# Kernel tuning notes

Measured on AMD Instinct MI355X. Metric: run time of the kernel, lower is better.

## Reference

```python
import jax, jax.numpy as jnp
from jax import lax
import numpy as np

NPOINT, RADIUS, NSAMPLE = 1024, 0.2, 32
MLP = [64, 64, 128]
IN_CH = 35  # 3 coord channels + 32 point features
EPS = 1e-5


def farthest_point_sample(xyz, npoint):
    # xyz: (B, N, 3) -> (B, npoint) int32. Deterministic start at index 0.
    B, N, _ = xyz.shape

    def step(carry, _):
        dist, farthest = carry  # (B,N), (B,)
        centroid = jnp.take_along_axis(xyz, farthest[:, None, None], axis=1)  # (B,1,3)
        d = jnp.sum((xyz - centroid) ** 2, axis=-1)  # (B,N)
        dist = jnp.minimum(dist, d)
        nxt = jnp.argmax(dist, axis=-1).astype(jnp.int32)
        return (dist, nxt), farthest

    init = (jnp.full((B, N), 1e10, xyz.dtype), jnp.zeros((B,), jnp.int32))
    _, idxs = lax.scan(step, init, None, length=npoint)
    return idxs.T  # (B, npoint)


def gather_points(points, idx):
    # points: (B, N, C); idx: (B, ...) int -> (B, ..., C)
    return jax.vmap(lambda p, i: p[i])(points, idx)


def query_ball_point(radius, nsample, xyz, new_xyz):
    # xyz: (B,N,3), new_xyz: (B,S,3) -> (B,S,nsample) int32
    B, N, _ = xyz.shape
    sqrdists = jnp.sum((new_xyz[:, :, None, :] - xyz[:, None, :, :]) ** 2, axis=-1)  # (B,S,N)
    group_idx = jnp.where(sqrdists > radius ** 2, N, jnp.arange(N, dtype=jnp.int32))
    group_idx = jnp.sort(group_idx, axis=-1)[:, :, :nsample]
    first = group_idx[:, :, :1]
    return jnp.where(group_idx == N, first, group_idx)


def sa_forward(xyz, points, params):
    B, N, C = xyz.shape
    fps_idx = farthest_point_sample(xyz, NPOINT)
    new_xyz = gather_points(xyz, fps_idx)  # (B,S,3)
    idx = query_ball_point(RADIUS, NSAMPLE, xyz, new_xyz)  # (B,S,K)
    grouped_xyz = gather_points(xyz, idx)  # (B,S,K,3)
    grouped_xyz_norm = grouped_xyz - new_xyz[:, :, None, :]
    grouped_points = gather_points(points, idx)  # (B,S,K,D)
    new_points = jnp.concatenate([grouped_xyz_norm, grouped_points], axis=-1)  # (B,S,K,Cin)
    x = new_points.transpose(0, 3, 2, 1)  # (B, Cin, K, S)
    for w, b, g, be in params:
        x = jnp.einsum('oi,biks->boks', w, x) + b[None, :, None, None]  # 1x1 conv
        mean = x.mean(axis=(0, 2, 3), keepdims=True)  # BatchNorm2d, training mode
        var = x.var(axis=(0, 2, 3), keepdims=True)
        x = (x - mean) / jnp.sqrt(var + EPS)
        x = jax.nn.relu(g[None, :, None, None] * x + be[None, :, None, None])
    new_points_out = x.max(axis=2)  # max over nsample -> (B, Cout, S)
    return new_xyz, new_points_out


def setup_inputs() -> dict:
    key = jax.random.key(0)
    ks = jax.random.split(key, 16)
    B, N, D = 16, 4096, 32
    inp = {
        'xyz': jax.random.uniform(ks[0], (B, N, 3), dtype=jnp.float32),
        'points': jax.random.normal(ks[1], (B, N, D), dtype=jnp.float32),
    }
    last = IN_CH
    for li, out_ch in enumerate(MLP):
        inp[f'w{li}'] = jax.random.normal(ks[2 + 4 * li], (out_ch, last), dtype=jnp.float32) * 0.05
        inp[f'b{li}'] = jnp.zeros((out_ch,), jnp.float32)
        inp[f'g{li}'] = jnp.ones((out_ch,), jnp.float32)
        inp[f'be{li}'] = jnp.zeros((out_ch,), jnp.float32)
        last = out_ch
    return inp


def reference(xyz, points, w0, b0, g0, be0, w1, b1, g1, be1, w2, b2, g2, be2):
    params = [(w0, b0, g0, be0), (w1, b1, g1, be1), (w2, b2, g2, be2)]
    return sa_forward(xyz, points, params)
```

## Files before the change

### kernel.cpp

```cpp
#include <hip/hip_runtime.h>
#include <hip/hip_bf16.h>
#include <stdint.h>

#pragma clang fp contract(off)

#define BATCH   16
#define NPTS    4096
#define NPOINT  1024
#define NSAMPLE 32
#define NPOS    (BATCH*NPOINT*NSAMPLE)
#define NBLK    (NPOS/128)
#define EPSV    1e-5f

typedef unsigned short ushort_t;
typedef unsigned int uint_t;
typedef unsigned long long u64;
typedef __attribute__((ext_vector_type(8))) short bf16x8;
typedef __attribute__((ext_vector_type(4))) float f32x4;
typedef __attribute__((ext_vector_type(2))) float f32x2;

__device__ inline ushort_t f2bf(float f) {
    uint_t u = __float_as_uint(f);
    u += 0x7fffu + ((u >> 16) & 1u);
    return (ushort_t)(u >> 16);
}
__device__ inline uint_t pkbf(float a, float b) {
    __hip_bfloat162 h = __float22bfloat162_rn(make_float2(a, b));
    uint_t r; __builtin_memcpy(&r, &h, 4); return r;
}
__device__ inline bf16x8 asbf(uint4 u) {
    bf16x8 v; __builtin_memcpy(&v, &u, 16); return v;
}
__device__ inline void unpack8(uint4 u, float* f) {
    f[0] = __uint_as_float(u.x << 16); f[1] = __uint_as_float(u.x & 0xffff0000u);
    f[2] = __uint_as_float(u.y << 16); f[3] = __uint_as_float(u.y & 0xffff0000u);
    f[4] = __uint_as_float(u.z << 16); f[5] = __uint_as_float(u.z & 0xffff0000u);
    f[6] = __uint_as_float(u.w << 16); f[7] = __uint_as_float(u.w & 0xffff0000u);
}

__global__ __launch_bounds__(256) void prep_w(const float* __restrict__ w0,
                                              const float* __restrict__ w1,
                                              const float* __restrict__ w2,
                                              ushort_t* __restrict__ Wp0,
                                              ushort_t* __restrict__ Wx0,
                                              ushort_t* __restrict__ Wp1,
                                              ushort_t* __restrict__ Wp2) {
    const int t = blockIdx.x * 256 + threadIdx.x;
    const int stride = gridDim.x * 256;
    for (int i = t; i < 64 * 32; i += stride) { int ch = i >> 5, k = i & 31; Wp0[i] = f2bf(w0[ch * 35 + 3 + k]); }
    for (int i = t; i < 64 * 4;  i += stride) { int ch = i >> 2, q = i & 3;  Wx0[i] = (q < 3) ? f2bf(w0[ch * 35 + q]) : (ushort_t)0; }
    for (int i = t; i < 64 * 64; i += stride) Wp1[i] = f2bf(w1[i]);
    for (int i = t; i < 128 * 64; i += stride) Wp2[i] = f2bf(w2[i]);
}

#define DPP_MAX_STAGE(CTRL) do {                                              \
    uint_t _lo2 = __builtin_amdgcn_update_dpp(lo, lo, CTRL, 0xf, 0xf, false); \
    uint_t _hi2 = __builtin_amdgcn_update_dpp(hi, hi, CTRL, 0xf, 0xf, false); \
    u64 _o = ((u64)_hi2 << 32) | _lo2;                                        \
    u64 _v = ((u64)hi << 32) | lo;                                            \
    bool _g = _o > _v;                                                        \
    lo = _g ? _lo2 : lo; hi = _g ? _hi2 : hi;                                 \
} while (0)

__global__ __launch_bounds__(256) void fps_kernel(const float* __restrict__ xyz,
                                                  float* __restrict__ new_xyz) {
    __shared__ float4 lxyz[NPTS];
    __shared__ u64 wbest[2][4];
    __shared__ int fpsidx[NPOINT];
    const int b = blockIdx.x;
    const int tid = threadIdx.x;
    const float* base = xyz + (size_t)b * NPTS * 3;
    for (int n = tid; n < NPTS; n += 256) {
        lxyz[n] = make_float4(base[3 * n], base[3 * n + 1], base[3 * n + 2], 0.f);
    }
    __syncthreads();

    f32x2 px[8], py[8], pz[8], dist[8];
    uint_t lowc[16];
#pragma unroll
    for (int j = 0; j < 8; j++) {
        float4 v0 = lxyz[tid + (2 * j) * 256];
        float4 v1 = lxyz[tid + (2 * j + 1) * 256];
        px[j] = (f32x2){v0.x, v1.x};
        py[j] = (f32x2){v0.y, v1.y};
        pz[j] = (f32x2){v0.z, v1.z};
        dist[j] = (f32x2){1e10f, 1e10f};
        lowc[2 * j] = ~(uint_t)(tid + (2 * j) * 256);
        lowc[2 * j + 1] = ~(uint_t)(tid + (2 * j + 1) * 256);
    }
    if (tid == 0) fpsidx[0] = 0;
    int cur = 0;
    const int lane = tid & 63, wid = tid >> 6;

    for (int it = 1; it < NPOINT; ++it) {
        float4 c = lxyz[cur];
        const f32x2 cx = (f32x2){c.x, c.x};
        const f32x2 cy = (f32x2){c.y, c.y};
        const f32x2 cz = (f32x2){c.z, c.z};
        u64 t[8];
#pragma unroll
        for (int j = 0; j < 8; j++) {
            f32x2 dx = px[j] - cx;
            f32x2 dy = py[j] - cy;
            f32x2 dz = pz[j] - cz;
            f32x2 d = (dx * dx + dy * dy) + dz * dz;
            f32x2 nd = __builtin_elementwise_min(dist[j], d);
            dist[j] = nd;
            u64 e0 = ((u64)__float_as_uint(nd.x) << 32) | lowc[2 * j];
            u64 e1 = ((u64)__float_as_uint(nd.y) << 32) | lowc[2 * j + 1];
            t[j] = e0 > e1 ? e0 : e1;
        }
#pragma unroll
        for (int j = 0; j < 4; j++) { u64 o = t[j + 4]; t[j] = t[j] > o ? t[j] : o; }
        t[0] = t[0] > t[1] ? t[0] : t[1];
        t[2] = t[2] > t[3] ? t[2] : t[3];
        u64 v = t[0] > t[2] ? t[0] : t[2];

        uint_t lo = (uint_t)v, hi = (uint_t)(v >> 32);
        DPP_MAX_STAGE(0x111);
        DPP_MAX_STAGE(0x112);
        DPP_MAX_STAGE(0x114);
        DPP_MAX_STAGE(0x118);
        DPP_MAX_STAGE(0x142);
        DPP_MAX_STAGE(0x143);
        uint_t mlo = __builtin_amdgcn_readlane(lo, 63);
        uint_t mhi = __builtin_amdgcn_readlane(hi, 63);

        const int par = it & 1;
        if (lane == 0) wbest[par][wid] = ((u64)mhi << 32) | mlo;
        __syncthreads();
        u64 b0 = wbest[par][0], b1 = wbest[par][1];
        u64 b2 = wbest[par][2], b3 = wbest[par][3];
        u64 m01 = b0 > b1 ? b0 : b1;
        u64 m23 = b2 > b3 ? b2 : b3;
        u64 bb = m01 > m23 ? m01 : m23;
        cur = (int)(~(uint_t)bb) & (NPTS - 1);
        if (tid == 0) fpsidx[it] = cur;
    }
    __syncthreads();
    float* ob = new_xyz + (size_t)b * NPOINT * 3;
    for (int s = tid; s < NPOINT; s += 256) {
        float4 v = lxyz[fpsidx[s]];
        ob[3 * s + 0] = v.x; ob[3 * s + 1] = v.y; ob[3 * s + 2] = v.z;
    }
}

__global__ __launch_bounds__(256) void ballq_kernel(const float* __restrict__ xyz,
                                                    const float* __restrict__ new_xyz,
                                                    int* __restrict__ gidx) {
    const int gw = (int)((blockIdx.x * 256 + threadIdx.x) >> 6);
    const int lane = threadIdx.x & 63;
    const int b = gw / NPOINT, s = gw % NPOINT;
    const float* nb = new_xyz + ((size_t)b * NPOINT + s) * 3;
    const float cx = nb[0], cy = nb[1], cz = nb[2];
    const float* xb = xyz + (size_t)b * NPTS * 3;
    const float r2 = (float)(0.2 * 0.2);
    int cnt = 0;
    int first = -1;
    int* out = gidx + (size_t)gw * NSAMPLE;
    for (int j0 = 0; j0 < NPTS; j0 += 64) {
        int j = j0 + lane;
        float dx = __fsub_rn(xb[j * 3 + 0], cx);
        float dy = __fsub_rn(xb[j * 3 + 1], cy);
        float dz = __fsub_rn(xb[j * 3 + 2], cz);
        float d = __fadd_rn(__fadd_rn(__fmul_rn(dx, dx), __fmul_rn(dy, dy)),
                            __fmul_rn(dz, dz));
        bool pred = !(d > r2);
        u64 mask = __ballot(pred);
        if (first < 0 && mask != 0ull) first = j0 + (__ffsll((long long)mask) - 1);
        int before = __popcll(mask & ((1ull << lane) - 1ull));
        int slot = cnt + before;
        if (pred && slot < NSAMPLE) out[slot] = j;
        cnt += (int)__popcll(mask);
        if (cnt >= NSAMPLE) break;
    }
    if (cnt < NSAMPLE) {
        if (lane >= cnt && lane < NSAMPLE) out[lane] = first;
    }
}

__global__ __launch_bounds__(256) void conv1_mfma(const float* __restrict__ xyz,
                                                  const float* __restrict__ points,
                                                  const float* __restrict__ new_xyz,
                                                  const int* __restrict__ gidx,
                                                  const ushort_t* __restrict__ Wp0,
                                                  const ushort_t* __restrict__ Wx0,
                                                  const float* __restrict__ bias,
                                                  ushort_t* __restrict__ Y,
                                                  float* __restrict__ part_s,
                                                  float* __restrict__ part_q) {
    const int lane = threadIdx.x & 63, wid = threadIdx.x >> 6;
    const int l15 = lane & 15, quad = lane >> 4;
    const int p0 = blockIdx.x * 128 + wid * 32;

    bf16x8 Bp[4], Bx[4];
#pragma unroll
    for (int nt = 0; nt < 4; nt++) {
        const int ch = nt * 16 + l15;
        Bp[nt] = *(const bf16x8*)(Wp0 + (size_t)ch * 32 + quad * 8);
        uint4 bx = {0u, 0u, 0u, 0u};
        if (quad == 0) {
            uint2 wv = *(const uint2*)(Wx0 + ch * 4);
            bx.x = wv.x; bx.y = wv.y;
        }
        Bx[nt] = asbf(bx);
    }
    f32x4 acc[2][4];
#pragma unroll
    for (int mt = 0; mt < 2; mt++)
#pragma unroll
        for (int nt = 0; nt < 4; nt++) acc[mt][nt] = (f32x4){0.f, 0.f, 0.f, 0.f};

#pragma unroll
    for (int mt = 0; mt < 2; mt++) {
        const int p = p0 + mt * 16 + l15;
        const int b = p >> 15, s = (p & 32767) >> 5;
        const int j = gidx[p];
        const float* pr = points + ((size_t)(b * NPTS + j)) * 32 + quad * 8;
        float4 pa = *(const float4*)pr;
        float4 pb4 = *(const float4*)(pr + 4);
        uint4 ap;
        ap.x = pkbf(pa.x, pa.y);  ap.y = pkbf(pa.z, pa.w);
        ap.z = pkbf(pb4.x, pb4.y); ap.w = pkbf(pb4.z, pb4.w);
        bf16x8 Ap = asbf(ap);
        uint4 ax = {0u, 0u, 0u, 0u};
        if (quad == 0) {
            const float* xp = xyz + ((size_t)(b * NPTS + j)) * 3;
            const float* nz = new_xyz + ((size_t)(b * NPOINT + s)) * 3;
            float d0 = xp[0] - nz[0], d1 = xp[1] - nz[1], d2 = xp[2] - nz[2];
            ax.x = pkbf(d0, d1);
            ax.y = pkbf(d2, 0.f);
        }
        bf16x8 Ax = asbf(ax);
#pragma unroll
        for (int nt = 0; nt < 4; nt++) {
            acc[mt][nt] = __builtin_amdgcn_mfma_f32_16x16x32_bf16(Ap, Bp[nt], acc[mt][nt], 0, 0, 0);
            acc[mt][nt] = __builtin_amdgcn_mfma_f32_16x16x32_bf16(Ax, Bx[nt], acc[mt][nt], 0, 0, 0);
        }
    }
    float s_[4], q_[4];
#pragma unroll
    for (int nt = 0; nt < 4; nt++) { s_[nt] = 0.f; q_[nt] = 0.f; }
#pragma unroll
    for (int nt = 0; nt < 4; nt++) {
        const int ch = nt * 16 + l15;
        const float bs = bias[ch];
#pragma unroll
        for (int mt = 0; mt < 2; mt++) {
            const int pb = p0 + mt * 16 + quad * 4;
            float x0 = acc[mt][nt][0] + bs, x1 = acc[mt][nt][1] + bs;
            float x2 = acc[mt][nt][2] + bs, x3 = acc[mt][nt][3] + bs;
            uint_t p01 = pkbf(x0, x1), p23 = pkbf(x2, x3);
            Y[(size_t)(pb + 0) * 64 + ch] = (ushort_t)(p01 & 0xffffu);
            Y[(size_t)(pb + 1) * 64 + ch] = (ushort_t)(p01 >> 16);
            Y[(size_t)(pb + 2) * 64 + ch] = (ushort_t)(p23 & 0xffffu);
            Y[(size_t)(pb + 3) * 64 + ch] = (ushort_t)(p23 >> 16);
            float v0 = __uint_as_float(p01 << 16), v1 = __uint_as_float(p01 & 0xffff0000u);
            float v2 = __uint_as_float(p23 << 16), v3 = __uint_as_float(p23 & 0xffff0000u);
            s_[nt] += (v0 + v1) + (v2 + v3);
            q_[nt] += (v0 * v0 + v1 * v1) + (v2 * v2 + v3 * v3);
        }
    }
#pragma unroll
    for (int nt = 0; nt < 4; nt++) {
        s_[nt] += __shfl_xor(s_[nt], 16, 64); s_[nt] += __shfl_xor(s_[nt], 32, 64);
        q_[nt] += __shfl_xor(q_[nt], 16, 64); q_[nt] += __shfl_xor(q_[nt], 32, 64);
    }
    __shared__ float reds[4][4][16], redq[4][4][16];
    if (lane < 16) {
#pragma unroll
        for (int nt = 0; nt < 4; nt++) { reds[wid][nt][lane] = s_[nt]; redq[wid][nt][lane] = q_[nt]; }
    }
    __syncthreads();
    if (threadIdx.x < 16) {
#pragma unroll
        for (int nt = 0; nt < 4; nt++) {
            float ss = 0.f, qq = 0.f;
#pragma unroll
            for (int w = 0; w < 4; w++) { ss += reds[w][nt][threadIdx.x]; qq += redq[w][nt][threadIdx.x]; }
            const int ch = nt * 16 + threadIdx.x;
            part_s[(size_t)ch * NBLK + blockIdx.x] = ss;
            part_q[(size_t)ch * NBLK + blockIdx.x] = qq;
        }
    }
}

template <int IN, int OUT>
__global__ __launch_bounds__(256) void convN_mfma(const ushort_t* __restrict__ Yin,
                                                  const float* __restrict__ scale,
                                                  const float* __restrict__ shift,
                                                  const ushort_t* __restrict__ Wp,
                                                  const float* __restrict__ bias,
                                                  ushort_t* __restrict__ Yout,
                                                  float* __restrict__ part_s,
                                                  float* __restrict__ part_q) {
    constexpr int NT = OUT / 16;
    const int lane = threadIdx.x & 63, wid = threadIdx.x >> 6;
    const int l15 = lane & 15, quad = lane >> 4;
    const int p0 = blockIdx.x * 128 + wid * 32;

    float sc[2][8], sh[2][8];
#pragma unroll
    for (int kq = 0; kq < 2; kq++) {
        const int i0 = kq * 32 + quad * 8;
        float4 a0 = *(const float4*)(scale + i0);
        float4 a1 = *(const float4*)(scale + i0 + 4);
        float4 b0v = *(const float4*)(shift + i0);
        float4 b1v = *(const float4*)(shift + i0 + 4);
        sc[kq][0] = a0.x; sc[kq][1] = a0.y; sc[kq][2] = a0.z; sc[kq][3] = a0.w;
        sc[kq][4] = a1.x; sc[kq][5] = a1.y; sc[kq][6] = a1.z; sc[kq][7] = a1.w;
        sh[kq][0] = b0v.x; sh[kq][1] = b0v.y; sh[kq][2] = b0v.z; sh[kq][3] = b0v.w;
        sh[kq][4] = b1v.x; sh[kq][5] = b1v.y; sh[kq][6] = b1v.z; sh[kq][7] = b1v.w;
    }
    bf16x8 Bf[NT][2];
#pragma unroll
    for (int nt = 0; nt < NT; nt++)
#pragma unroll
        for (int kq = 0; kq < 2; kq++)
            Bf[nt][kq] = *(const bf16x8*)(Wp + (size_t)(nt * 16 + l15) * IN + kq * 32 + quad * 8);

    bf16x8 Af[2][2];
#pragma unroll
    for (int mt = 0; mt < 2; mt++)
#pragma unroll
        for (int kq = 0; kq < 2; kq++) {
            const ushort_t* yr = Yin + (size_t)(p0 + mt * 16 + l15) * IN + kq * 32 + quad * 8;
            uint4 u = *(const uint4*)yr;
            float f[8]; unpack8(u, f);
            float g0 = fmaxf(fmaf(f[0], sc[kq][0], sh[kq][0]), 0.f);
            float g1 = fmaxf(fmaf(f[1], sc[kq][1], sh[kq][1]), 0.f);
            float g2 = fmaxf(fmaf(f[2], sc[kq][2], sh[kq][2]), 0.f);
            float g3 = fmaxf(fmaf(f[3], sc[kq][3], sh[kq][3]), 0.f);
            float g4 = fmaxf(fmaf(f[4], sc[kq][4], sh[kq][4]), 0.f);
            float g5 = fmaxf(fmaf(f[5], sc[kq][5], sh[kq][5]), 0.f);
            float g6 = fmaxf(fmaf(f[6], sc[kq][6], sh[kq][6]), 0.f);
            float g7 = fmaxf(fmaf(f[7], sc[kq][7], sh[kq][7]), 0.f);
            uint4 a;
            a.x = pkbf(g0, g1); a.y = pkbf(g2, g3);
            a.z = pkbf(g4, g5); a.w = pkbf(g6, g7);
            Af[mt][kq] = asbf(a);
        }

    f32x4 acc[2][NT];
#pragma unroll
    for (int mt = 0; mt < 2; mt++)
#pragma unroll
        for (int nt = 0; nt < NT; nt++) acc[mt][nt] = (f32x4){0.f, 0.f, 0.f, 0.f};
#pragma unroll
    for (int mt = 0; mt < 2; mt++)
#pragma unroll
        for (int nt = 0; nt < NT; nt++) {
            acc[mt][nt] = __builtin_amdgcn_mfma_f32_16x16x32_bf16(Af[mt][0], Bf[nt][0], acc[mt][nt], 0, 0, 0);
            acc[mt][nt] = __builtin_amdgcn_mfma_f32_16x16x32_bf16(Af[mt][1], Bf[nt][1], acc[mt][nt], 0, 0, 0);
        }
    float s_[NT], q_[NT];
#pragma unroll
    for (int nt = 0; nt < NT; nt++) { s_[nt] = 0.f; q_[nt] = 0.f; }
#pragma unroll
    for (int nt = 0; nt < NT; nt++) {
        const int ch = nt * 16 + l15;
        const float bs = bias[ch];
#pragma unroll
        for (int mt = 0; mt < 2; mt++) {
            const int pb = p0 + mt * 16 + quad * 4;
            float x0 = acc[mt][nt][0] + bs, x1 = acc[mt][nt][1] + bs;
            float x2 = acc[mt][nt][2] + bs, x3 = acc[mt][nt][3] + bs;
            uint_t p01 = pkbf(x0, x1), p23 = pkbf(x2, x3);
            Yout[(size_t)(pb + 0) * OUT + ch] = (ushort_t)(p01 & 0xffffu);
            Yout[(size_t)(pb + 1) * OUT + ch] = (ushort_t)(p01 >> 16);
            Yout[(size_t)(pb + 2) * OUT + ch] = (ushort_t)(p23 & 0xffffu);
            Yout[(size_t)(pb + 3) * OUT + ch] = (ushort_t)(p23 >> 16);
            float v0 = __uint_as_float(p01 << 16), v1 = __uint_as_float(p01 & 0xffff0000u);
            float v2 = __uint_as_float(p23 << 16), v3 = __uint_as_float(p23 & 0xffff0000u);
            s_[nt] += (v0 + v1) + (v2 + v3);
            q_[nt] += (v0 * v0 + v1 * v1) + (v2 * v2 + v3 * v3);
        }
    }
#pragma unroll
    for (int nt = 0; nt < NT; nt++) {
        s_[nt] += __shfl_xor(s_[nt], 16, 64); s_[nt] += __shfl_xor(s_[nt], 32, 64);
        q_[nt] += __shfl_xor(q_[nt], 16, 64); q_[nt] += __shfl_xor(q_[nt], 32, 64);
    }
    __shared__ float reds[4][NT][16], redq[4][NT][16];
    if (lane < 16) {
#pragma unroll
        for (int nt = 0; nt < NT; nt++) { reds[wid][nt][lane] = s_[nt]; redq[wid][nt][lane] = q_[nt]; }
    }
    __syncthreads();
    if (threadIdx.x < 16) {
#pragma unroll
        for (int nt = 0; nt < NT; nt++) {
            float ss = 0.f, qq = 0.f;
#pragma unroll
            for (int w = 0; w < 4; w++) { ss += reds[w][nt][threadIdx.x]; qq += redq[w][nt][threadIdx.x]; }
            const int ch = nt * 16 + threadIdx.x;
            part_s[(size_t)ch * NBLK + blockIdx.x] = ss;
            part_q[(size_t)ch * NBLK + blockIdx.x] = qq;
        }
    }
}

__global__ __launch_bounds__(256) void reduce_finalize(const float* __restrict__ part_s,
                                                       const float* __restrict__ part_q,
                                                       const float* __restrict__ g,
                                                       const float* __restrict__ be,
                                                       float* __restrict__ scale,
                                                       float* __restrict__ shift) {
    const int ch = blockIdx.x;
    const float* p1 = part_s + (size_t)ch * NBLK;
    const float* p2 = part_q + (size_t)ch * NBLK;
    float s = 0.f, q = 0.f;
    for (int i = threadIdx.x; i < NBLK; i += 256) { s += p1[i]; q += p2[i]; }
#pragma unroll
    for (int m = 1; m < 64; m <<= 1) { s += __shfl_xor(s, m, 64); q += __shfl_xor(q, m, 64); }
    __shared__ float ls[4], lq[4];
    const int lane = threadIdx.x & 63, wid = threadIdx.x >> 6;
    if (lane == 0) { ls[wid] = s; lq[wid] = q; }
    __syncthreads();
    if (threadIdx.x == 0) {
        float ssum = ls[0] + ls[1] + ls[2] + ls[3];
        float qsum = lq[0] + lq[1] + lq[2] + lq[3];
        float mean = ssum * (1.f / (float)NPOS);
        float var = qsum * (1.f / (float)NPOS) - mean * mean;
        float inv = 1.f / sqrtf(var + EPSV);
        float sc = g[ch] * inv;
        scale[ch] = sc;
        shift[ch] = be[ch] - mean * sc;
    }
}

__global__ __launch_bounds__(256) void final_kernel(const ushort_t* __restrict__ Y3,
                                                    const float* __restrict__ scale,
                                                    const float* __restrict__ shift,
                                                    float* __restrict__ out) {
    const int b = blockIdx.x >> 5;
    const int stile = (blockIdx.x & 31) * 32;
    const int sl = threadIdx.x >> 3;
    const int oc = threadIdx.x & 7;
    const int s = stile + sl;
    const size_t base = ((size_t)(b * NPOINT + s)) * 32 * 128 + oc * 16;
    float vmax[16];
#pragma unroll
    for (int i = 0; i < 16; i++) vmax[i] = 0.f;
    for (int k = 0; k < 32; k++) {
        const ushort_t* yp = Y3 + base + (size_t)k * 128;
#pragma unroll
        for (int h = 0; h < 2; h++) {
            uint4 u = *(const uint4*)(yp + h * 8);
            float f[8];
            unpack8(u, f);
#pragma unroll
            for (int i = 0; i < 8; i++) {
                int o = oc * 16 + h * 8 + i;
                float v = fmaf(f[i], scale[o], shift[o]);
                vmax[h * 8 + i] = fmaxf(vmax[h * 8 + i], v);
            }
        }
    }
    __shared__ float res[32][130];
#pragma unroll
    for (int i = 0; i < 16; i++) res[sl][oc * 16 + i] = vmax[i];
    __syncthreads();
    const int so = threadIdx.x & 31;
    const int og = threadIdx.x >> 5;
#pragma unroll
    for (int r = 0; r < 16; r++) {
        int o = og * 16 + r;
        out[((size_t)(b * 128 + o)) * NPOINT + stile + so] = res[so][o];
    }
}

extern "C" void kernel_launch(void* const* d_in, const int* in_sizes, int n_in,
                              void* d_out, int out_size, void* d_ws, size_t ws_size,
                              hipStream_t stream) {
    const float* xyz = (const float*)d_in[0];
    const float* points = (const float*)d_in[1];
    const float* w0 = (const float*)d_in[2];
    const float* b0 = (const float*)d_in[3];
    const float* g0 = (const float*)d_in[4];
    const float* be0 = (const float*)d_in[5];
    const float* w1 = (const float*)d_in[6];
    const float* b1 = (const float*)d_in[7];
    const float* g1 = (const float*)d_in[8];
    const float* be1 = (const float*)d_in[9];
    const float* w2 = (const float*)d_in[10];
    const float* b2 = (const float*)d_in[11];
    const float* g2 = (const float*)d_in[12];
    const float* be2 = (const float*)d_in[13];

    float* out = (float*)d_out;
    float* new_xyz = out;
    float* final_out = out + BATCH * NPOINT * 3;

    char* ws = (char*)d_ws;
    const size_t MB = 1024u * 1024u;
    const size_t o_gidx = 0;
    const size_t o_y2 = 2 * MB;
    const size_t o_y13 = o_y2 + (size_t)NPOS * 64 * 2;
    const size_t o_params = o_y13 + (size_t)NPOS * 128 * 2;
    const size_t o_parts = o_params + 4096;
    const size_t o_w = o_parts + 4 * MB;

    int* gidx = (int*)(ws + o_gidx);
    ushort_t* Y1 = (ushort_t*)(ws + o_y13);
    ushort_t* Y2 = (ushort_t*)(ws + o_y2);
    ushort_t* Y3 = (ushort_t*)(ws + o_y13);
    float* pr = (float*)(ws + o_params);
    float* scale1 = pr + 0, *shift1 = pr + 64;
    float* scale2 = pr + 128, *shift2 = pr + 192;
    float* scale3 = pr + 256, *shift3 = pr + 384;
    float* part_s = (float*)(ws + o_parts);
    float* part_q = part_s + (size_t)128 * NBLK;
    ushort_t* Wp0 = (ushort_t*)(ws + o_w);
    ushort_t* Wx0 = Wp0 + 64 * 32;
    ushort_t* Wp1 = Wx0 + 64 * 4;
    ushort_t* Wp2 = Wp1 + 64 * 64;

    prep_w<<<8, 256, 0, stream>>>(w0, w1, w2, Wp0, Wx0, Wp1, Wp2);
    fps_kernel<<<BATCH, 256, 0, stream>>>(xyz, new_xyz);
    ballq_kernel<<<(BATCH * NPOINT) / 4, 256, 0, stream>>>(xyz, new_xyz, gidx);
    conv1_mfma<<<NBLK, 256, 0, stream>>>(xyz, points, new_xyz, gidx, Wp0, Wx0, b0, Y1, part_s, part_q);
    reduce_finalize<<<64, 256, 0, stream>>>(part_s, part_q, g0, be0, scale1, shift1);
    convN_mfma<64, 64><<<NBLK, 256, 0, stream>>>(Y1, scale1, shift1, Wp1, b1, Y2, part_s, part_q);
    reduce_finalize<<<64, 256, 0, stream>>>(part_s, part_q, g1, be1, scale2, shift2);
    convN_mfma<64, 128><<<NBLK, 256, 0, stream>>>(Y2, scale2, shift2, Wp2, b2, Y3, part_s, part_q);
    reduce_finalize<<<128, 256, 0, stream>>>(part_s, part_q, g2, be2, scale3, shift3);
    final_kernel<<<BATCH * 32, 256, 0, stream>>>(Y3, scale3, shift3, final_out);
}
```

Before: 909.6 us.

## Fuse group max/min into conv3 to avoid writing full layer-3 activations

The third conv kernel now reduces each 32-sample group to a per-channel max and min of the pre-BatchNorm output, instead of writing the full bf16 activation tensor. The final kernel picks max or min depending on the sign of the BN scale, then applies the affine transform and ReLU. This removes a large 128-channel intermediate write and its read-back, at the cost of two smaller fp32 max/min buffers and extra shuffles in conv3. Results can differ slightly because max/min are taken on fp32 values rather than bf16-rounded ones.

```diff
diff --git a/kernel.cpp b/kernel.cpp
--- a/kernel.cpp
+++ b/kernel.cpp
@@ -10,6 +10,7 @@
 #define NSAMPLE 32
 #define NPOS    (BATCH*NPOINT*NSAMPLE)
 #define NBLK    (NPOS/128)
+#define NGRP    (BATCH*NPOINT)
 #define EPSV    1e-5f
 
 typedef unsigned short ushort_t;
@@ -285,8 +286,7 @@
     }
 }
 
-template <int IN, int OUT>
-__global__ __launch_bounds__(256) void convN_mfma(const ushort_t* __restrict__ Yin,
+__global__ __launch_bounds__(256) void conv2_mfma(const ushort_t* __restrict__ Yin,
                                                   const float* __restrict__ scale,
                                                   const float* __restrict__ shift,
                                                   const ushort_t* __restrict__ Wp,
@@ -294,7 +294,7 @@
                                                   ushort_t* __restrict__ Yout,
                                                   float* __restrict__ part_s,
                                                   float* __restrict__ part_q) {
-    constexpr int NT = OUT / 16;
+    constexpr int IN = 64, OUT = 64, NT = 4;
     const int lane = threadIdx.x & 63, wid = threadIdx.x >> 6;
     const int l15 = lane & 15, quad = lane >> 4;
     const int p0 = blockIdx.x * 128 + wid * 32;
@@ -303,14 +303,8 @@
 #pragma unroll
     for (int kq = 0; kq < 2; kq++) {
         const int i0 = kq * 32 + quad * 8;
-        float4 a0 = *(const float4*)(scale + i0);
-        float4 a1 = *(const float4*)(scale + i0 + 4);
-        float4 b0v = *(const float4*)(shift + i0);
-        float4 b1v = *(const float4*)(shift + i0 + 4);
-        sc[kq][0] = a0.x; sc[kq][1] = a0.y; sc[kq][2] = a0.z; sc[kq][3] = a0.w;
-        sc[kq][4] = a1.x; sc[kq][5] = a1.y; sc[kq][6] = a1.z; sc[kq][7] = a1.w;
-        sh[kq][0] = b0v.x; sh[kq][1] = b0v.y; sh[kq][2] = b0v.z; sh[kq][3] = b0v.w;
-        sh[kq][4] = b1v.x; sh[kq][5] = b1v.y; sh[kq][6] = b1v.z; sh[kq][7] = b1v.w;
+#pragma unroll
+        for (int q = 0; q < 8; q++) { sc[kq][q] = scale[i0 + q]; sh[kq][q] = shift[i0 + q]; }
     }
     bf16x8 Bf[NT][2];
 #pragma unroll
@@ -400,6 +394,121 @@
     }
 }
 
+__global__ __launch_bounds__(256) void conv3_mfma(const ushort_t* __restrict__ Yin,
+                                                  const float* __restrict__ scale,
+                                                  const float* __restrict__ shift,
+                                                  const ushort_t* __restrict__ Wp,
+                                                  const float* __restrict__ bias,
+                                                  float* __restrict__ xmax,
+                                                  float* __restrict__ xmin,
+                                                  float* __restrict__ part_s,
+                                                  float* __restrict__ part_q) {
+    constexpr int IN = 64, NT = 8;
+    const int lane = threadIdx.x & 63, wid = threadIdx.x >> 6;
+    const int l15 = lane & 15, quad = lane >> 4;
+    const int p0 = blockIdx.x * 128 + wid * 32;
+    const int g = p0 >> 5;
+
+    float sc[2][8], sh[2][8];
+#pragma unroll
+    for (int kq = 0; kq < 2; kq++) {
+        const int i0 = kq * 32 + quad * 8;
+#pragma unroll
+        for (int q = 0; q < 8; q++) { sc[kq][q] = scale[i0 + q]; sh[kq][q] = shift[i0 + q]; }
+    }
+    bf16x8 Bf[NT][2];
+#pragma unroll
+    for (int nt = 0; nt < NT; nt++)
+#pragma unroll
+        for (int kq = 0; kq < 2; kq++)
+            Bf[nt][kq] = *(const bf16x8*)(Wp + (size_t)(nt * 16 + l15) * IN + kq * 32 + quad * 8);
+
+    bf16x8 Af[2][2];
+#pragma unroll
+    for (int mt = 0; mt < 2; mt++)
+#pragma unroll
+        for (int kq = 0; kq < 2; kq++) {
+            const ushort_t* yr = Yin + (size_t)(p0 + mt * 16 + l15) * IN + kq * 32 + quad * 8;
+            uint4 u = *(const uint4*)yr;
+            float f[8]; unpack8(u, f);
+            float g0 = fmaxf(fmaf(f[0], sc[kq][0], sh[kq][0]), 0.f);
+            float g1 = fmaxf(fmaf(f[1], sc[kq][1], sh[kq][1]), 0.f);
+            float g2 = fmaxf(fmaf(f[2], sc[kq][2], sh[kq][2]), 0.f);
+            float g3 = fmaxf(fmaf(f[3], sc[kq][3], sh[kq][3]), 0.f);
+            float g4 = fmaxf(fmaf(f[4], sc[kq][4], sh[kq][4]), 0.f);
+            float g5 = fmaxf(fmaf(f[5], sc[kq][5], sh[kq][5]), 0.f);
+            float g6 = fmaxf(fmaf(f[6], sc[kq][6], sh[kq][6]), 0.f);
+            float g7 = fmaxf(fmaf(f[7], sc[kq][7], sh[kq][7]), 0.f);
+            uint4 a;
+            a.x = pkbf(g0, g1); a.y = pkbf(g2, g3);
+            a.z = pkbf(g4, g5); a.w = pkbf(g6, g7);
+            Af[mt][kq] = asbf(a);
+        }
+
+    f32x4 acc[2][NT];
+#pragma unroll
+    for (int mt = 0; mt < 2; mt++)
+#pragma unroll
+        for (int nt = 0; nt < NT; nt++) acc[mt][nt] = (f32x4){0.f, 0.f, 0.f, 0.f};
+#pragma unroll
+    for (int mt = 0; mt < 2; mt++)
+#pragma unroll
+        for (int nt = 0; nt < NT; nt++) {
+            acc[mt][nt] = __builtin_amdgcn_mfma_f32_16x16x32_bf16(Af[mt][0], Bf[nt][0], acc[mt][nt], 0, 0, 0);
+            acc[mt][nt] = __builtin_amdgcn_mfma_f32_16x16x32_bf16(Af[mt][1], Bf[nt][1], acc[mt][nt], 0, 0, 0);
+        }
+    float s_[NT], q_[NT], xm[NT], xn[NT];
+#pragma unroll
+    for (int nt = 0; nt < NT; nt++) { s_[nt] = 0.f; q_[nt] = 0.f; xm[nt] = -3e38f; xn[nt] = 3e38f; }
+#pragma unroll
+    for (int nt = 0; nt < NT; nt++) {
+        const float bs = bias[nt * 16 + l15];
+#pragma unroll
+        for (int mt = 0; mt < 2; mt++) {
+#pragma unroll
+            for (int r = 0; r < 4; r++) {
+                float x = acc[mt][nt][r] + bs;
+                s_[nt] += x; q_[nt] += x * x;
+                xm[nt] = fmaxf(xm[nt], x); xn[nt] = fminf(xn[nt], x);
+            }
+        }
+    }
+#pragma unroll
+    for (int nt = 0; nt < NT; nt++) {
+        s_[nt] += __shfl_xor(s_[nt], 16, 64); s_[nt] += __shfl_xor(s_[nt], 32, 64);
+        q_[nt] += __shfl_xor(q_[nt], 16, 64); q_[nt] += __shfl_xor(q_[nt], 32, 64);
+        xm[nt] = fmaxf(xm[nt], __shfl_xor(xm[nt], 16, 64));
+        xm[nt] = fmaxf(xm[nt], __shfl_xor(xm[nt], 32, 64));
+        xn[nt] = fminf(xn[nt], __shfl_xor(xn[nt], 16, 64));
+        xn[nt] = fminf(xn[nt], __shfl_xor(xn[nt], 32, 64));
+    }
+    if (quad == 0) {
+#pragma unroll
+        for (int nt = 0; nt < NT; nt++) {
+            const int ch = nt * 16 + l15;
+            xmax[(size_t)g * 128 + ch] = xm[nt];
+            xmin[(size_t)g * 128 + ch] = xn[nt];
+        }
+    }
+    __shared__ float reds[4][NT][16], redq[4][NT][16];
+    if (lane < 16) {
+#pragma unroll
+        for (int nt = 0; nt < NT; nt++) { reds[wid][nt][lane] = s_[nt]; redq[wid][nt][lane] = q_[nt]; }
+    }
+    __syncthreads();
+    if (threadIdx.x < 16) {
+#pragma unroll
+        for (int nt = 0; nt < NT; nt++) {
+            float ss = 0.f, qq = 0.f;
+#pragma unroll
+            for (int w = 0; w < 4; w++) { ss += reds[w][nt][threadIdx.x]; qq += redq[w][nt][threadIdx.x]; }
+            const int ch = nt * 16 + threadIdx.x;
+            part_s[(size_t)ch * NBLK + blockIdx.x] = ss;
+            part_q[(size_t)ch * NBLK + blockIdx.x] = qq;
+        }
+    }
+}
+
 __global__ __launch_bounds__(256) void reduce_finalize(const float* __restrict__ part_s,
                                                        const float* __restrict__ part_q,
                                                        const float* __restrict__ g,
@@ -429,44 +538,28 @@
     }
 }
 
-__global__ __launch_bounds__(256) void final_kernel(const ushort_t* __restrict__ Y3,
-                                                    const float* __restrict__ scale,
-                                                    const float* __restrict__ shift,
-                                                    float* __restrict__ out) {
-    const int b = blockIdx.x >> 5;
-    const int stile = (blockIdx.x & 31) * 32;
-    const int sl = threadIdx.x >> 3;
-    const int oc = threadIdx.x & 7;
-    const int s = stile + sl;
-    const size_t base = ((size_t)(b * NPOINT + s)) * 32 * 128 + oc * 16;
-    float vmax[16];
-#pragma unroll
-    for (int i = 0; i < 16; i++) vmax[i] = 0.f;
-    for (int k = 0; k < 32; k++) {
-        const ushort_t* yp = Y3 + base + (size_t)k * 128;
-#pragma unroll
-        for (int h = 0; h < 2; h++) {
-            uint4 u = *(const uint4*)(yp + h * 8);
-            float f[8];
-            unpack8(u, f);
-#pragma unroll
-            for (int i = 0; i < 8; i++) {
-                int o = oc * 16 + h * 8 + i;
-                float v = fmaf(f[i], scale[o], shift[o]);
-                vmax[h * 8 + i] = fmaxf(vmax[h * 8 + i], v);
-            }
-        }
-    }
-    __shared__ float res[32][130];
-#pragma unroll
-    for (int i = 0; i < 16; i++) res[sl][oc * 16 + i] = vmax[i];
+__global__ __launch_bounds__(256) void final2_kernel(const float* __restrict__ xmax,
+                                                     const float* __restrict__ xmin,
+                                                     const float* __restrict__ scale,
+                                                     const float* __restrict__ shift,
+                                                     float* __restrict__ out) {
+    __shared__ float buf[128][129];
+    const int b = blockIdx.x >> 3;
+    const int s0 = (blockIdx.x & 7) * 128;
+    const int tid = threadIdx.x;
+    for (int i = tid; i < 128 * 128; i += 256) {
+        const int si = i >> 7, ch = i & 127;
+        const size_t g = (size_t)(b * NPOINT + s0 + si);
+        const float sc = scale[ch], sh = shift[ch];
+        const float xM = xmax[g * 128 + ch];
+        const float xN = xmin[g * 128 + ch];
+        const float X = sc > 0.f ? xM : xN;
+        buf[si][ch] = fmaxf(fmaf(X, sc, sh), 0.f);
+    }
     __syncthreads();
-    const int so = threadIdx.x & 31;
-    const int og = threadIdx.x >> 5;
-#pragma unroll
-    for (int r = 0; r < 16; r++) {
-        int o = og * 16 + r;
-        out[((size_t)(b * 128 + o)) * NPOINT + stile + so] = res[so][o];
+    for (int i = tid; i < 128 * 128; i += 256) {
+        const int ch = i >> 7, si = i & 127;
+        out[((size_t)(b * 128 + ch)) * NPOINT + s0 + si] = buf[si][ch];
     }
 }
 
@@ -496,15 +589,16 @@
     const size_t MB = 1024u * 1024u;
     const size_t o_gidx = 0;
     const size_t o_y2 = 2 * MB;
-    const size_t o_y13 = o_y2 + (size_t)NPOS * 64 * 2;
-    const size_t o_params = o_y13 + (size_t)NPOS * 128 * 2;
+    const size_t o_y1 = o_y2 + (size_t)NPOS * 64 * 2;
+    const size_t o_params = o_y1 + (size_t)NPOS * 64 * 2;
     const size_t o_parts = o_params + 4096;
     const size_t o_w = o_parts + 4 * MB;
+    const size_t o_xm = o_w + 64 * 1024;
+    const size_t o_xn = o_xm + (size_t)NGRP * 128 * 4;
 
     int* gidx = (int*)(ws + o_gidx);
-    ushort_t* Y1 = (ushort_t*)(ws + o_y13);
+    ushort_t* Y1 = (ushort_t*)(ws + o_y1);
     ushort_t* Y2 = (ushort_t*)(ws + o_y2);
-    ushort_t* Y3 = (ushort_t*)(ws + o_y13);
     float* pr = (float*)(ws + o_params);
     float* scale1 = pr + 0, *shift1 = pr + 64;
     float* scale2 = pr + 128, *shift2 = pr + 192;
@@ -515,15 +609,17 @@
     ushort_t* Wx0 = Wp0 + 64 * 32;
     ushort_t* Wp1 = Wx0 + 64 * 4;
     ushort_t* Wp2 = Wp1 + 64 * 64;
+    float* xmax = (float*)(ws + o_xm);
+    float* xmin = (float*)(ws + o_xn);
 
     prep_w<<<8, 256, 0, stream>>>(w0, w1, w2, Wp0, Wx0, Wp1, Wp2);
     fps_kernel<<<BATCH, 256, 0, stream>>>(xyz, new_xyz);
     ballq_kernel<<<(BATCH * NPOINT) / 4, 256, 0, stream>>>(xyz, new_xyz, gidx);
     conv1_mfma<<<NBLK, 256, 0, stream>>>(xyz, points, new_xyz, gidx, Wp0, Wx0, b0, Y1, part_s, part_q);
     reduce_finalize<<<64, 256, 0, stream>>>(part_s, part_q, g0, be0, scale1, shift1);
-    convN_mfma<64, 64><<<NBLK, 256, 0, stream>>>(Y1, scale1, shift1, Wp1, b1, Y2, part_s, part_q);
+    conv2_mfma<<<NBLK, 256, 0, stream>>>(Y1, scale1, shift1, Wp1, b1, Y2, part_s, part_q);
     reduce_finalize<<<64, 256, 0, stream>>>(part_s, part_q, g1, be1, scale2, shift2);
-    convN_mfma<64, 128><<<NBLK, 256, 0, stream>>>(Y2, scale2, shift2, Wp2, b2, Y3, part_s, part_q);
+    conv3_mfma<<<NBLK, 256, 0, stream>>>(Y2, scale2, shift2, Wp2, b2, xmax, xmin, part_s, part_q);
     reduce_finalize<<<128, 256, 0, stream>>>(part_s, part_q, g2, be2, scale3, shift3);
-    final_kernel<<<BATCH * 32, 256, 0, stream>>>(Y3, scale3, shift3, final_out);
-}
+    final2_kernel<<<128, 256, 0, stream>>>(xmax, xmin, scale3, shift3, final_out);
+}
```

After: 890.9 us. -2.1%, faster.
